# Kernel tuning notes

Measured on AMD Instinct MI355X. Metric: run time of the kernel, lower is better.

The kernel has to match this reference:

```python
import jax, jax.numpy as jnp
import numpy as np

HIDDEN = 1024
NUM_EXPERTS = 8
TOP_K = 2


def setup_inputs() -> dict:
    key = jax.random.key(0)
    k_x, k_r, k_w1, k_w2 = jax.random.split(key, 4)
    x = jax.random.normal(k_x, (4, 2048, HIDDEN), dtype=jnp.float32)
    # router: nn.Linear(hidden, num_experts, bias=False) -> weight [E, H]
    router_w = jax.random.normal(k_r, (NUM_EXPERTS, HIDDEN), dtype=jnp.float32) * (HIDDEN ** -0.5)
    # expert FFN: Linear(H, 2H) then Linear(2H, H), stored as [E, H, 2H] and [E, 2H, H]
    w1 = jax.random.normal(k_w1, (NUM_EXPERTS, HIDDEN, 2 * HIDDEN), dtype=jnp.float32) * (HIDDEN ** -0.5)
    w2 = jax.random.normal(k_w2, (NUM_EXPERTS, 2 * HIDDEN, HIDDEN), dtype=jnp.float32) * ((2 * HIDDEN) ** -0.5)
    return {"x": x, "router_w": router_w, "w1": w1, "w2": w2}


def reference(x, router_w, w1, w2):
    bsz, seq, hidden = x.shape
    tokens = x.reshape(-1, hidden)                      # [T, H]
    logits = tokens @ router_w.T                        # [T, E]
    topk_vals, topk_idx = jax.lax.top_k(logits, TOP_K)  # [T, K]
    weights = jax.nn.softmax(topk_vals, axis=-1)        # [T, K]
    # Dense all-experts FFN (exact GELU, matching torch nn.GELU default)
    h = jnp.einsum('td,edf->etf', tokens, w1)           # [E, T, 2H]
    h = jax.nn.gelu(h, approximate=False)
    out_all = jnp.einsum('etf,efd->etd', h, w2)         # [E, T, H]
    # Gather top-k expert outputs per token and weighted-combine
    out_ted = jnp.transpose(out_all, (1, 0, 2))         # [T, E, H]
    gathered = jnp.take_along_axis(out_ted, topk_idx[:, :, None], axis=1)  # [T, K, H]
    output = jnp.sum(weights[:, :, None] * gathered, axis=1)               # [T, H]
    return output.reshape(bsz, seq, hidden)
```

## Files before the change

kernel.cpp:

```cpp
#include <hip/hip_runtime.h>
#include <cstdint>
#include <cstddef>

#define T_TOKENS 8192
#define HID 1024
#define HID2 2048
#define NE 8

typedef unsigned short u16;
typedef unsigned int u32;
typedef __bf16 bf16x8 __attribute__((ext_vector_type(8)));
typedef float f32x4 __attribute__((ext_vector_type(4)));

__device__ __forceinline__ float bf2f(u16 u) {
    union { u32 i; float f; } x; x.i = ((u32)u) << 16; return x.f;
}
__device__ __forceinline__ u16 f2bf(float f) {
    union { float f; u32 i; } x; x.f = f;
    u32 r = x.i + 0x7fffu + ((x.i >> 16) & 1u);
    return (u16)(r >> 16);
}

__device__ __forceinline__ void cp16(const void* g, void* l) {
    __builtin_amdgcn_global_load_lds(
        (const __attribute__((address_space(1))) u32*)g,
        (__attribute__((address_space(3))) u32*)l,
        16, 0, 0);
}

__device__ __forceinline__ float gelu_f(float v) {
    float v2 = v * v;
    float t = fmaf(0.0713548162726f, v2, 1.59576912161f);
    float d = 1.0f + __expf(-v * t);
    return v * __builtin_amdgcn_rcpf(d);
}

__global__ __launch_bounds__(256) void router_kernel(
    const float* __restrict__ x, const float* __restrict__ rw,
    u16* __restrict__ xb,
    int* __restrict__ cnt, int* __restrict__ rowlist,
    int* __restrict__ tok_slots, float* __restrict__ tok_w)
{
    __shared__ int lbin[NE];
    __shared__ int gbase[NE];
    int tid = threadIdx.x;
    if (tid < NE) lbin[tid] = 0;
    __syncthreads();

    int wave = tid >> 6;
    int lane = tid & 63;
    int tg = lane >> 3, il = lane & 7;
    int t = blockIdx.x * 32 + wave * 8 + tg;

    const float* xrow = x + (size_t)t * HID;
    u16* xbrow = xb + (size_t)t * HID;

    float acc[NE];
#pragma unroll
    for (int e = 0; e < NE; e++) acc[e] = 0.f;

#pragma unroll 8
    for (int q = 0; q < 32; q++) {
        int c = il * 4 + 32 * q;
        float4 xv = *(const float4*)(xrow + c);
        u16 p[4] = { f2bf(xv.x), f2bf(xv.y), f2bf(xv.z), f2bf(xv.w) };
        *(uint2*)(xbrow + c) = *(const uint2*)p;
#pragma unroll
        for (int e = 0; e < NE; e++) {
            float4 rv = *(const float4*)(rw + (size_t)e * HID + c);
            acc[e] = fmaf(xv.x, rv.x, acc[e]);
            acc[e] = fmaf(xv.y, rv.y, acc[e]);
            acc[e] = fmaf(xv.z, rv.z, acc[e]);
            acc[e] = fmaf(xv.w, rv.w, acc[e]);
        }
    }
#pragma unroll
    for (int e = 0; e < NE; e++) {
        acc[e] += __shfl_xor(acc[e], 1, 64);
        acc[e] += __shfl_xor(acc[e], 2, 64);
        acc[e] += __shfl_xor(acc[e], 4, 64);
    }

    int i0 = 0, i1 = 0, ph0 = 0, ph1 = 0;
    float w0 = 0.f, w1 = 0.f;
    if (il == 0) {
        float v0 = -1e30f;
#pragma unroll
        for (int e = 0; e < NE; e++) if (acc[e] > v0) { v0 = acc[e]; i0 = e; }
        float v1 = -1e30f;
#pragma unroll
        for (int e = 0; e < NE; e++) if (e != i0 && acc[e] > v1) { v1 = acc[e]; i1 = e; }
        w0 = 1.0f / (1.0f + __expf(v1 - v0));
        w1 = 1.0f - w0;
        ph0 = atomicAdd(&lbin[i0], 1);
        ph1 = atomicAdd(&lbin[i1], 1);
    }
    __syncthreads();
    if (tid < NE) gbase[tid] = atomicAdd(&cnt[tid * 32], lbin[tid]);
    __syncthreads();
    if (il == 0) {
        int p0 = gbase[i0] + ph0;
        int p1 = gbase[i1] + ph1;
        rowlist[i0 * T_TOKENS + p0] = t;
        rowlist[i1 * T_TOKENS + p1] = t;
        tok_slots[t * 2 + 0] = (i0 << 16) | p0;
        tok_slots[t * 2 + 1] = (i1 << 16) | p1;
        tok_w[t * 2 + 0] = w0;
        tok_w[t * 2 + 1] = w1;
    }
}

__global__ void offsets_kernel(const int* __restrict__ cnt,
                               int* __restrict__ off, int* __restrict__ cntc)
{
    if (threadIdx.x == 0) {
        int s = 0;
        for (int e = 0; e < NE; e++) {
            int c = cnt[e * 32];
            off[e] = s; cntc[e] = c; s += c;
        }
    }
}

__global__ __launch_bounds__(256) void convtrans_kernel(
    const float* __restrict__ in, u16* __restrict__ outp, int K, int N)
{
    __shared__ u16 tile[64][72];
    int e = blockIdx.z;
    const float* ip = in + (size_t)e * K * N;
    u16* op = outp + (size_t)e * K * N;
    int n0 = blockIdx.x * 64, k0 = blockIdx.y * 64;
    int t = threadIdx.x;

    int k = t >> 2;
    int nq = (t & 3) * 16;
    const float* src = ip + (size_t)(k0 + k) * N + n0 + nq;
#pragma unroll
    for (int q = 0; q < 4; q++) {
        float4 v = *(const float4*)(src + q * 4);
        tile[nq + q * 4 + 0][k] = f2bf(v.x);
        tile[nq + q * 4 + 1][k] = f2bf(v.y);
        tile[nq + q * 4 + 2][k] = f2bf(v.z);
        tile[nq + q * 4 + 3][k] = f2bf(v.w);
    }
    __syncthreads();

    int n = t >> 2;
    int kq = (t & 3) * 16;
    u16* dst = op + (size_t)(n0 + n) * K + k0 + kq;
    *(uint4*)(dst + 0) = *(const uint4*)&tile[n][kq + 0];
    *(uint4*)(dst + 8) = *(const uint4*)&tile[n][kq + 8];
}

#define BM 128
#define BN 128
#define BK 64

__global__ __launch_bounds__(256) void gemm1_kernel(
    const u16* __restrict__ xb, const u16* __restrict__ w1t,
    const int* __restrict__ cntc, const int* __restrict__ off,
    const int* __restrict__ rowlist, u16* __restrict__ hbuf)
{
    int e = blockIdx.z;
    int n_e = cntc[e];
    int mt = blockIdx.x;
    if (mt * BM >= n_e) return;
    int nt = blockIdx.y;

    __shared__ u16 As[BM * BK];
    __shared__ u16 Bs[BN * BK];
    __shared__ int toks[BM];

    int tid = threadIdx.x;
    if (tid < BM) {
        int r = mt * BM + tid;
        toks[tid] = (r < n_e) ? rowlist[e * T_TOKENS + r] : 0;
    }
    __syncthreads();

    int wv = tid >> 6, lane = tid & 63;
    int wm = (wv & 1) * 64, wn = (wv >> 1) * 64;
    int l15 = lane & 15, l4 = lane >> 4;
    int sr = lane >> 3, sc = lane & 7;

    const u16* w1e = w1t + ((size_t)e * HID2 + nt * BN) * HID;

    const u16* aptr[4]; const u16* bptr[4];
    u16* adst[4]; u16* bdst[4];
#pragma unroll
    for (int i = 0; i < 4; i++) {
        int m = wv * 32 + i * 8 + sr;
        int gq = sc ^ (m & 7);
        aptr[i] = xb + (size_t)toks[m] * HID + gq * 8;
        adst[i] = &As[m * BK + sc * 8];
        bptr[i] = w1e + (size_t)m * HID + gq * 8;
        bdst[i] = &Bs[m * BK + sc * 8];
    }

    f32x4 acc[4][4];
#pragma unroll
    for (int i = 0; i < 4; i++)
#pragma unroll
        for (int j = 0; j < 4; j++) acc[i][j] = (f32x4){0.f, 0.f, 0.f, 0.f};

    for (int kb = 0; kb < HID; kb += BK) {
#pragma unroll
        for (int i = 0; i < 4; i++) {
            cp16(aptr[i] + kb, adst[i]);
            cp16(bptr[i] + kb, bdst[i]);
        }
        __syncthreads();
#pragma unroll
        for (int ks = 0; ks < 2; ks++) {
            bf16x8 af[4], bfr[4];
            int q = ks * 4 + l4;
#pragma unroll
            for (int i = 0; i < 4; i++) {
                int ra = wm + i * 16 + l15;
                af[i] = *(const bf16x8*)&As[ra * BK + ((q ^ (ra & 7)) << 3)];
                int rb = wn + i * 16 + l15;
                bfr[i] = *(const bf16x8*)&Bs[rb * BK + ((q ^ (rb & 7)) << 3)];
            }
#pragma unroll
            for (int i = 0; i < 4; i++)
#pragma unroll
                for (int j = 0; j < 4; j++)
                    acc[i][j] = __builtin_amdgcn_mfma_f32_16x16x32_bf16(bfr[j], af[i], acc[i][j], 0, 0, 0);
        }
        __syncthreads();
    }

    int base_row = off[e] + mt * BM;
#pragma unroll
    for (int i = 0; i < 4; i++) {
        int m = wm + i * 16 + l15;
        int r = mt * BM + m;
        if (r < n_e) {
            u16* orow = hbuf + (size_t)(base_row + m) * HID2 + nt * BN + wn + l4 * 4;
#pragma unroll
            for (int j = 0; j < 4; j++) {
                u16 p[4];
#pragma unroll
                for (int rg = 0; rg < 4; rg++) p[rg] = f2bf(gelu_f(acc[i][j][rg]));
                *(uint2*)(orow + j * 16) = *(const uint2*)p;
            }
        }
    }
}

__global__ __launch_bounds__(256) void gemm2_kernel(
    const u16* __restrict__ hbuf, const u16* __restrict__ w2t,
    const int* __restrict__ cntc, const int* __restrict__ off,
    u16* __restrict__ ybuf)
{
    int e = blockIdx.z;
    int n_e = cntc[e];
    int mt = blockIdx.x;
    if (mt * BM >= n_e) return;
    int nt = blockIdx.y;

    __shared__ u16 As[BM * BK];
    __shared__ u16 Bs[BN * BK];

    int tid = threadIdx.x;
    int wv = tid >> 6, lane = tid & 63;
    int wm = (wv & 1) * 64, wn = (wv >> 1) * 64;
    int l15 = lane & 15, l4 = lane >> 4;
    int sr = lane >> 3, sc = lane & 7;

    const u16* hrow = hbuf + (size_t)(off[e] + mt * BM) * HID2;
    const u16* w2e = w2t + ((size_t)e * HID + nt * BN) * HID2;

    const u16* aptr[4]; const u16* bptr[4];
    u16* adst[4]; u16* bdst[4];
#pragma unroll
    for (int i = 0; i < 4; i++) {
        int m = wv * 32 + i * 8 + sr;
        int gq = sc ^ (m & 7);
        aptr[i] = hrow + (size_t)m * HID2 + gq * 8;
        adst[i] = &As[m * BK + sc * 8];
        bptr[i] = w2e + (size_t)m * HID2 + gq * 8;
        bdst[i] = &Bs[m * BK + sc * 8];
    }

    f32x4 acc[4][4];
#pragma unroll
    for (int i = 0; i < 4; i++)
#pragma unroll
        for (int j = 0; j < 4; j++) acc[i][j] = (f32x4){0.f, 0.f, 0.f, 0.f};

    for (int kb = 0; kb < HID2; kb += BK) {
#pragma unroll
        for (int i = 0; i < 4; i++) {
            cp16(aptr[i] + kb, adst[i]);
            cp16(bptr[i] + kb, bdst[i]);
        }
        __syncthreads();
#pragma unroll
        for (int ks = 0; ks < 2; ks++) {
            bf16x8 af[4], bfr[4];
            int q = ks * 4 + l4;
#pragma unroll
            for (int i = 0; i < 4; i++) {
                int ra = wm + i * 16 + l15;
                af[i] = *(const bf16x8*)&As[ra * BK + ((q ^ (ra & 7)) << 3)];
                int rb = wn + i * 16 + l15;
                bfr[i] = *(const bf16x8*)&Bs[rb * BK + ((q ^ (rb & 7)) << 3)];
            }
#pragma unroll
            for (int i = 0; i < 4; i++)
#pragma unroll
                for (int j = 0; j < 4; j++)
                    acc[i][j] = __builtin_amdgcn_mfma_f32_16x16x32_bf16(bfr[j], af[i], acc[i][j], 0, 0, 0);
        }
        __syncthreads();
    }

    int base_row = off[e] + mt * BM;
#pragma unroll
    for (int i = 0; i < 4; i++) {
        int m = wm + i * 16 + l15;
        int r = mt * BM + m;
        if (r < n_e) {
            u16* orow = ybuf + (size_t)(base_row + m) * HID + nt * BN + wn + l4 * 4;
#pragma unroll
            for (int j = 0; j < 4; j++) {
                u16 p[4];
#pragma unroll
                for (int rg = 0; rg < 4; rg++) p[rg] = f2bf(acc[i][j][rg]);
                *(uint2*)(orow + j * 16) = *(const uint2*)p;
            }
        }
    }
}

__global__ __launch_bounds__(256) void combine_kernel(
    const u16* __restrict__ ybuf, const int* __restrict__ off,
    const int* __restrict__ tok_slots, const float* __restrict__ tok_w,
    float* __restrict__ out)
{
    int tid = threadIdx.x;
    int t = blockIdx.x * 2 + (tid >> 7);
    int c = (tid & 127) * 8;
    int s0 = tok_slots[t * 2], s1 = tok_slots[t * 2 + 1];
    float w0 = tok_w[t * 2], w1 = tok_w[t * 2 + 1];
    int r0 = off[s0 >> 16] + (s0 & 0xFFFF);
    int r1 = off[s1 >> 16] + (s1 & 0xFFFF);
    uint4 a = *(const uint4*)(ybuf + (size_t)r0 * HID + c);
    uint4 b = *(const uint4*)(ybuf + (size_t)r1 * HID + c);
    const u16* pa = (const u16*)&a;
    const u16* pb = (const u16*)&b;
    float o[8];
#pragma unroll
    for (int q = 0; q < 8; q++) o[q] = w0 * bf2f(pa[q]) + w1 * bf2f(pb[q]);
    *(float4*)(out + (size_t)t * HID + c) = *(const float4*)&o[0];
    *(float4*)(out + (size_t)t * HID + c + 4) = *(const float4*)&o[4];
}

extern "C" void kernel_launch(void* const* d_in, const int* in_sizes, int n_in,
                              void* d_out, int out_size, void* d_ws, size_t ws_size,
                              hipStream_t stream)
{
    const float* x  = (const float*)d_in[0];
    const float* rw = (const float*)d_in[1];
    const float* w1 = (const float*)d_in[2];
    const float* w2 = (const float*)d_in[3];
    float* out = (float*)d_out;

    char* ws = (char*)d_ws;
    int*   cnt       = (int*)(ws + 0);
    int*   off       = (int*)(ws + 1024);
    int*   cntc      = (int*)(ws + 1088);
    int*   rowlist   = (int*)(ws + 2048);
    int*   tok_slots = (int*)(ws + 2048 + 262144);
    float* tok_w     = (float*)(ws + 2048 + 262144 + 65536);
    u16*   xb        = (u16*)(ws + (1ull << 20));
    u16*   wt        = (u16*)(ws + (17ull << 20));
    u16*   hbuf      = (u16*)(ws + (49ull << 20));
    u16*   ybuf      = (u16*)(ws + (114ull << 20));

    hipMemsetAsync(cnt, 0, 1024, stream);

    router_kernel<<<T_TOKENS / 32, 256, 0, stream>>>(x, rw, xb, cnt, rowlist, tok_slots, tok_w);
    offsets_kernel<<<1, 64, 0, stream>>>(cnt, off, cntc);

    convtrans_kernel<<<dim3(HID2 / 64, HID / 64, NE), 256, 0, stream>>>(w1, wt, HID, HID2);
    gemm1_kernel<<<dim3(T_TOKENS / BM, HID2 / BN, NE), 256, 0, stream>>>(xb, wt, cntc, off, rowlist, hbuf);

    convtrans_kernel<<<dim3(HID / 64, HID2 / 64, NE), 256, 0, stream>>>(w2, wt, HID2, HID);
    gemm2_kernel<<<dim3(T_TOKENS / BM, HID / BN, NE), 256, 0, stream>>>(hbuf, wt, cntc, off, ybuf);

    combine_kernel<<<T_TOKENS / 2, 256, 0, stream>>>(ybuf, off, tok_slots, tok_w, out);
}
```

Before: 548.0 us.

## Use 256x256 double-buffered expert GEMM tiles with compact tile map

```diff
diff --git a/kernel.cpp b/kernel.cpp
--- a/kernel.cpp
+++ b/kernel.cpp
@@ -110,15 +110,24 @@
     }
 }
 
+#define BM 256
+#define BN 256
+#define BK 64
+#define LDSE (BM * BK)
+
 __global__ void offsets_kernel(const int* __restrict__ cnt,
-                               int* __restrict__ off, int* __restrict__ cntc)
+                               int* __restrict__ off, int* __restrict__ cntc,
+                               int* __restrict__ tmap, int* __restrict__ ntile)
 {
     if (threadIdx.x == 0) {
-        int s = 0;
+        int s = 0, ti = 0;
         for (int e = 0; e < NE; e++) {
             int c = cnt[e * 32];
             off[e] = s; cntc[e] = c; s += c;
-        }
+            int nmt = (c + BM - 1) / BM;
+            for (int m = 0; m < nmt; m++) tmap[ti++] = (e << 16) | m;
+        }
+        ntile[0] = ti;
     }
 }
 
@@ -152,34 +161,33 @@
     *(uint4*)(dst + 8) = *(const uint4*)&tile[n][kq + 8];
 }
 
-#define BM 128
-#define BN 128
-#define BK 64
-
-__global__ __launch_bounds__(256) void gemm1_kernel(
+__global__ __launch_bounds__(512, 2) void gemm1_kernel(
     const u16* __restrict__ xb, const u16* __restrict__ w1t,
     const int* __restrict__ cntc, const int* __restrict__ off,
-    const int* __restrict__ rowlist, u16* __restrict__ hbuf)
-{
-    int e = blockIdx.z;
+    const int* __restrict__ rowlist, const int* __restrict__ tmap,
+    const int* __restrict__ ntile, u16* __restrict__ hbuf)
+{
+    __shared__ u16 As[2][LDSE];
+    __shared__ u16 Bs[2][LDSE];
+    __shared__ int toks[BM];
+
+    int bt = blockIdx.x;
+    if (bt >= ntile[0]) return;
+    int em = tmap[bt];
+    int e = em >> 16, mt = em & 0xffff;
+    int nt = blockIdx.y;
     int n_e = cntc[e];
-    int mt = blockIdx.x;
-    if (mt * BM >= n_e) return;
-    int nt = blockIdx.y;
-
-    __shared__ u16 As[BM * BK];
-    __shared__ u16 Bs[BN * BK];
-    __shared__ int toks[BM];
 
     int tid = threadIdx.x;
     if (tid < BM) {
         int r = mt * BM + tid;
-        toks[tid] = (r < n_e) ? rowlist[e * T_TOKENS + r] : 0;
+        if (r >= n_e) r = n_e - 1;
+        toks[tid] = rowlist[e * T_TOKENS + r];
     }
     __syncthreads();
 
     int wv = tid >> 6, lane = tid & 63;
-    int wm = (wv & 1) * 64, wn = (wv >> 1) * 64;
+    int wm = (wv >> 2) * 128, wn = (wv & 3) * 64;
     int l15 = lane & 15, l4 = lane >> 4;
     int sr = lane >> 3, sc = lane & 7;
 
@@ -192,47 +200,65 @@
         int m = wv * 32 + i * 8 + sr;
         int gq = sc ^ (m & 7);
         aptr[i] = xb + (size_t)toks[m] * HID + gq * 8;
-        adst[i] = &As[m * BK + sc * 8];
+        adst[i] = &As[0][m * BK + sc * 8];
         bptr[i] = w1e + (size_t)m * HID + gq * 8;
-        bdst[i] = &Bs[m * BK + sc * 8];
-    }
-
-    f32x4 acc[4][4];
-#pragma unroll
-    for (int i = 0; i < 4; i++)
+        bdst[i] = &Bs[0][m * BK + sc * 8];
+    }
+
+    f32x4 acc[8][4];
+#pragma unroll
+    for (int i = 0; i < 8; i++)
 #pragma unroll
         for (int j = 0; j < 4; j++) acc[i][j] = (f32x4){0.f, 0.f, 0.f, 0.f};
 
-    for (int kb = 0; kb < HID; kb += BK) {
-#pragma unroll
-        for (int i = 0; i < 4; i++) {
-            cp16(aptr[i] + kb, adst[i]);
-            cp16(bptr[i] + kb, bdst[i]);
-        }
-        __syncthreads();
+#pragma unroll
+    for (int i = 0; i < 4; i++) { cp16(aptr[i], adst[i]); cp16(bptr[i], bdst[i]); }
+    asm volatile("s_waitcnt vmcnt(0)" ::: "memory");
+    __syncthreads();
+
+    int cur = 0;
+    for (int kt = 0; kt < HID / BK; kt++) {
+        if (kt + 1 < HID / BK) {
+            int kb = (kt + 1) * BK;
+            int bo = (cur ^ 1) * LDSE;
+#pragma unroll
+            for (int i = 0; i < 4; i++) {
+                cp16(aptr[i] + kb, adst[i] + bo);
+                cp16(bptr[i] + kb, bdst[i] + bo);
+            }
+        }
+        const u16* Ab = As[cur];
+        const u16* Bb = Bs[cur];
 #pragma unroll
         for (int ks = 0; ks < 2; ks++) {
-            bf16x8 af[4], bfr[4];
+            bf16x8 af[8], bfr[4];
             int q = ks * 4 + l4;
 #pragma unroll
-            for (int i = 0; i < 4; i++) {
+            for (int i = 0; i < 8; i++) {
                 int ra = wm + i * 16 + l15;
-                af[i] = *(const bf16x8*)&As[ra * BK + ((q ^ (ra & 7)) << 3)];
-                int rb = wn + i * 16 + l15;
-                bfr[i] = *(const bf16x8*)&Bs[rb * BK + ((q ^ (rb & 7)) << 3)];
-            }
-#pragma unroll
-            for (int i = 0; i < 4; i++)
+                af[i] = *(const bf16x8*)&Ab[ra * BK + ((q ^ (ra & 7)) << 3)];
+            }
+#pragma unroll
+            for (int j = 0; j < 4; j++) {
+                int rb = wn + j * 16 + l15;
+                bfr[j] = *(const bf16x8*)&Bb[rb * BK + ((q ^ (rb & 7)) << 3)];
+            }
+            __builtin_amdgcn_s_setprio(1);
+#pragma unroll
+            for (int i = 0; i < 8; i++)
 #pragma unroll
                 for (int j = 0; j < 4; j++)
                     acc[i][j] = __builtin_amdgcn_mfma_f32_16x16x32_bf16(bfr[j], af[i], acc[i][j], 0, 0, 0);
-        }
+            __builtin_amdgcn_s_setprio(0);
+        }
+        if (kt + 1 < HID / BK) asm volatile("s_waitcnt vmcnt(0)" ::: "memory");
         __syncthreads();
+        cur ^= 1;
     }
 
     int base_row = off[e] + mt * BM;
 #pragma unroll
-    for (int i = 0; i < 4; i++) {
+    for (int i = 0; i < 8; i++) {
         int m = wm + i * 16 + l15;
         int r = mt * BM + m;
         if (r < n_e) {
@@ -248,23 +274,25 @@
     }
 }
 
-__global__ __launch_bounds__(256) void gemm2_kernel(
+__global__ __launch_bounds__(512, 2) void gemm2_kernel(
     const u16* __restrict__ hbuf, const u16* __restrict__ w2t,
     const int* __restrict__ cntc, const int* __restrict__ off,
+    const int* __restrict__ tmap, const int* __restrict__ ntile,
     u16* __restrict__ ybuf)
 {
-    int e = blockIdx.z;
+    __shared__ u16 As[2][LDSE];
+    __shared__ u16 Bs[2][LDSE];
+
+    int bt = blockIdx.x;
+    if (bt >= ntile[0]) return;
+    int em = tmap[bt];
+    int e = em >> 16, mt = em & 0xffff;
+    int nt = blockIdx.y;
     int n_e = cntc[e];
-    int mt = blockIdx.x;
-    if (mt * BM >= n_e) return;
-    int nt = blockIdx.y;
-
-    __shared__ u16 As[BM * BK];
-    __shared__ u16 Bs[BN * BK];
 
     int tid = threadIdx.x;
     int wv = tid >> 6, lane = tid & 63;
-    int wm = (wv & 1) * 64, wn = (wv >> 1) * 64;
+    int wm = (wv >> 2) * 128, wn = (wv & 3) * 64;
     int l15 = lane & 15, l4 = lane >> 4;
     int sr = lane >> 3, sc = lane & 7;
 
@@ -278,47 +306,65 @@
         int m = wv * 32 + i * 8 + sr;
         int gq = sc ^ (m & 7);
         aptr[i] = hrow + (size_t)m * HID2 + gq * 8;
-        adst[i] = &As[m * BK + sc * 8];
+        adst[i] = &As[0][m * BK + sc * 8];
         bptr[i] = w2e + (size_t)m * HID2 + gq * 8;
-        bdst[i] = &Bs[m * BK + sc * 8];
-    }
-
-    f32x4 acc[4][4];
-#pragma unroll
-    for (int i = 0; i < 4; i++)
+        bdst[i] = &Bs[0][m * BK + sc * 8];
+    }
+
+    f32x4 acc[8][4];
+#pragma unroll
+    for (int i = 0; i < 8; i++)
 #pragma unroll
         for (int j = 0; j < 4; j++) acc[i][j] = (f32x4){0.f, 0.f, 0.f, 0.f};
 
-    for (int kb = 0; kb < HID2; kb += BK) {
-#pragma unroll
-        for (int i = 0; i < 4; i++) {
-            cp16(aptr[i] + kb, adst[i]);
-            cp16(bptr[i] + kb, bdst[i]);
-        }
-        __syncthreads();
+#pragma unroll
+    for (int i = 0; i < 4; i++) { cp16(aptr[i], adst[i]); cp16(bptr[i], bdst[i]); }
+    asm volatile("s_waitcnt vmcnt(0)" ::: "memory");
+    __syncthreads();
+
+    int cur = 0;
+    for (int kt = 0; kt < HID2 / BK; kt++) {
+        if (kt + 1 < HID2 / BK) {
+            int kb = (kt + 1) * BK;
+            int bo = (cur ^ 1) * LDSE;
+#pragma unroll
+            for (int i = 0; i < 4; i++) {
+                cp16(aptr[i] + kb, adst[i] + bo);
+                cp16(bptr[i] + kb, bdst[i] + bo);
+            }
+        }
+        const u16* Ab = As[cur];
+        const u16* Bb = Bs[cur];
 #pragma unroll
         for (int ks = 0; ks < 2; ks++) {
-            bf16x8 af[4], bfr[4];
+            bf16x8 af[8], bfr[4];
             int q = ks * 4 + l4;
 #pragma unroll
-            for (int i = 0; i < 4; i++) {
+            for (int i = 0; i < 8; i++) {
                 int ra = wm + i * 16 + l15;
-                af[i] = *(const bf16x8*)&As[ra * BK + ((q ^ (ra & 7)) << 3)];
-                int rb = wn + i * 16 + l15;
-                bfr[i] = *(const bf16x8*)&Bs[rb * BK + ((q ^ (rb & 7)) << 3)];
-            }
-#pragma unroll
-            for (int i = 0; i < 4; i++)
+                af[i] = *(const bf16x8*)&Ab[ra * BK + ((q ^ (ra & 7)) << 3)];
+            }
+#pragma unroll
+            for (int j = 0; j < 4; j++) {
+                int rb = wn + j * 16 + l15;
+                bfr[j] = *(const bf16x8*)&Bb[rb * BK + ((q ^ (rb & 7)) << 3)];
+            }
+            __builtin_amdgcn_s_setprio(1);
+#pragma unroll
+            for (int i = 0; i < 8; i++)
 #pragma unroll
                 for (int j = 0; j < 4; j++)
                     acc[i][j] = __builtin_amdgcn_mfma_f32_16x16x32_bf16(bfr[j], af[i], acc[i][j], 0, 0, 0);
-        }
+            __builtin_amdgcn_s_setprio(0);
+        }
+        if (kt + 1 < HID2 / BK) asm volatile("s_waitcnt vmcnt(0)" ::: "memory");
         __syncthreads();
+        cur ^= 1;
     }
 
     int base_row = off[e] + mt * BM;
 #pragma unroll
-    for (int i = 0; i < 4; i++) {
+    for (int i = 0; i < 8; i++) {
         int m = wm + i * 16 + l15;
         int r = mt * BM + m;
         if (r < n_e) {
@@ -371,6 +417,8 @@
     int*   cnt       = (int*)(ws + 0);
     int*   off       = (int*)(ws + 1024);
     int*   cntc      = (int*)(ws + 1088);
+    int*   tmap      = (int*)(ws + 1152);
+    int*   ntile     = (int*)(ws + 1536);
     int*   rowlist   = (int*)(ws + 2048);
     int*   tok_slots = (int*)(ws + 2048 + 262144);
     float* tok_w     = (float*)(ws + 2048 + 262144 + 65536);
@@ -382,13 +430,13 @@
     hipMemsetAsync(cnt, 0, 1024, stream);
 
     router_kernel<<<T_TOKENS / 32, 256, 0, stream>>>(x, rw, xb, cnt, rowlist, tok_slots, tok_w);
-    offsets_kernel<<<1, 64, 0, stream>>>(cnt, off, cntc);
+    offsets_kernel<<<1, 64, 0, stream>>>(cnt, off, cntc, tmap, ntile);
 
     convtrans_kernel<<<dim3(HID2 / 64, HID / 64, NE), 256, 0, stream>>>(w1, wt, HID, HID2);
-    gemm1_kernel<<<dim3(T_TOKENS / BM, HID2 / BN, NE), 256, 0, stream>>>(xb, wt, cntc, off, rowlist, hbuf);
+    gemm1_kernel<<<dim3(72, HID2 / BN, 1), 512, 0, stream>>>(xb, wt, cntc, off, rowlist, tmap, ntile, hbuf);
 
     convtrans_kernel<<<dim3(HID / 64, HID2 / 64, NE), 256, 0, stream>>>(w2, wt, HID2, HID);
-    gemm2_kernel<<<dim3(T_TOKENS / BM, HID / BN, NE), 256, 0, stream>>>(hbuf, wt, cntc, off, ybuf);
+    gemm2_kernel<<<dim3(72, HID / BN, 1), 512, 0, stream>>>(hbuf, wt, cntc, off, tmap, ntile, ybuf);
 
     combine_kernel<<<T_TOKENS / 2, 256, 0, stream>>>(ybuf, off, tok_slots, tok_w, out);
 }
```

Result: faster. 485.0 us (-11.5%).
